# Kernel optimization log

Measured on AMD Instinct MI355X. Metric: run time of the kernel, lower is better.

The kernel has to match this reference:

```python
import jax, jax.numpy as jnp
import numpy as np

N_NODES = 50000


def _gcn_norm(edge_index, num_nodes):
    """Add self-loops and compute symmetric GCN normalization per edge.
    Returns (src, dst, norm) with src/dst of length E + N."""
    loop = jnp.arange(num_nodes, dtype=edge_index.dtype)
    src = jnp.concatenate([edge_index[0], loop])
    dst = jnp.concatenate([edge_index[1], loop])
    ones = jnp.ones(dst.shape[0], dtype=jnp.float32)
    deg = jax.ops.segment_sum(ones, dst, num_segments=num_nodes)
    dinv = jnp.where(deg > 0, jax.lax.rsqrt(deg), 0.0)
    norm = dinv[src] * dinv[dst]  # [E + N]
    return src, dst, norm


def _gcn_conv(x, src, dst, norm, W, b, num_nodes):
    h = x @ W                                # [N, out]
    msg = h[src] * norm[:, None]             # gather + scale, [E+N, out]
    out = jax.ops.segment_sum(msg, dst, num_segments=num_nodes)  # scatter-add
    return out + b


def setup_inputs() -> dict:
    key = jax.random.key(0)
    ks = jax.random.split(key, 10)
    F, H = 128, 128
    x = jax.random.normal(ks[0], (N_NODES, F), dtype=jnp.float32)
    edge_index = jax.random.randint(ks[1], (2, 800000), 0, N_NODES, dtype=jnp.int64)
    def glorot(k, fan_in, fan_out):
        s = (6.0 / (fan_in + fan_out)) ** 0.5
        return jax.random.uniform(k, (fan_in, fan_out), jnp.float32, -s, s)
    return {
        "x": x,
        "edge_index": edge_index,
        "W1": glorot(ks[2], F, H), "b1": jnp.zeros((H,), jnp.float32),
        "W2": glorot(ks[3], H, H), "b2": jnp.zeros((H,), jnp.float32),
        "W3": glorot(ks[4], H, H), "b3": jnp.zeros((H,), jnp.float32),
        "W4": glorot(ks[5], H, F), "b4": jnp.zeros((F,), jnp.float32),
    }


def reference(x, edge_index, W1, b1, W2, b2, W3, b3, W4, b4):
    n = x.shape[0]
    src, dst, norm = _gcn_norm(edge_index, n)  # same edges for all 4 layers
    h = jax.nn.relu(_gcn_conv(x, src, dst, norm, W1, b1, n))
    h = jax.nn.relu(_gcn_conv(h, src, dst, norm, W2, b2, n))
    h = jax.nn.relu(_gcn_conv(h, src, dst, norm, W3, b3, n))
    h = jax.nn.relu(_gcn_conv(h, src, dst, norm, W4, b4, n))
    return h
```

## Files before the change

kernel.cpp:

```cpp
#include <hip/hip_runtime.h>
#include <hip/hip_fp16.h>

typedef __attribute__((ext_vector_type(8))) _Float16 half8;
typedef __attribute__((ext_vector_type(4))) float f32x4;

static __device__ __forceinline__ half8 as_half8(uint4 u) {
    union { uint4 u; half8 h; } c; c.u = u; return c.h;
}


__global__ void prep_k(int* __restrict__ cnt, const float* __restrict__ x,
                       __half* __restrict__ Xh, int N) {
    int stride = gridDim.x * 256;
    int tid = blockIdx.x * 256 + threadIdx.x;
    for (int i = tid; i < 12544; i += stride) ((int4*)cnt)[i] = make_int4(0, 0, 0, 0);
    int nOut = N * 16;
    const float4* x4 = (const float4*)x;
    uint4* o4 = (uint4*)Xh;
    for (int i = tid; i < nOut; i += stride) {
        float4 f0 = x4[i * 2 + 0];
        float4 f1 = x4[i * 2 + 1];
        __half2 h0 = __floats2half2_rn(f0.x, f0.y);
        __half2 h1 = __floats2half2_rn(f0.z, f0.w);
        __half2 h2 = __floats2half2_rn(f1.x, f1.y);
        __half2 h3 = __floats2half2_rn(f1.z, f1.w);
        uint4 o;
        o.x = *(unsigned int*)&h0;
        o.y = *(unsigned int*)&h1;
        o.z = *(unsigned int*)&h2;
        o.w = *(unsigned int*)&h3;
        o4[i] = o;
    }
}

__global__ void hist_k(const int* __restrict__ dst, int* __restrict__ cnt, int E) {
    int e4 = blockIdx.x * 256 + threadIdx.x;
    int nE4 = E >> 2;
    if (e4 < nE4) {
        int4 d = ((const int4*)dst)[e4];
        atomicAdd(&cnt[d.x], 1);
        atomicAdd(&cnt[d.y], 1);
        atomicAdd(&cnt[d.z], 1);
        atomicAdd(&cnt[d.w], 1);
    } else if (e4 == nE4) {
        for (int e = nE4 * 4; e < E; ++e) atomicAdd(&cnt[dst[e]], 1);
    }
}

__global__ void bsum_k(const int* __restrict__ cnt, int* __restrict__ bsum,
                       float* __restrict__ dinv, int n) {
    int b = blockIdx.x, tid = threadIdx.x;
    int base = b * 1024 + tid * 4;
    int4 v = make_int4(0, 0, 0, 0);
    if (base + 3 < n) v = *(const int4*)(cnt + base);
    else {
        if (base + 0 < n) v.x = cnt[base + 0];
        if (base + 1 < n) v.y = cnt[base + 1];
        if (base + 2 < n) v.z = cnt[base + 2];
    }
    if (base + 3 < n) {
        float4 dv;
        dv.x = rsqrtf((float)v.x + 1.0f);
        dv.y = rsqrtf((float)v.y + 1.0f);
        dv.z = rsqrtf((float)v.z + 1.0f);
        dv.w = rsqrtf((float)v.w + 1.0f);
        *(float4*)(dinv + base) = dv;
    } else {
        if (base + 0 < n) dinv[base + 0] = rsqrtf((float)v.x + 1.0f);
        if (base + 1 < n) dinv[base + 1] = rsqrtf((float)v.y + 1.0f);
        if (base + 2 < n) dinv[base + 2] = rsqrtf((float)v.z + 1.0f);
    }
    int s = v.x + v.y + v.z + v.w;
#pragma unroll
    for (int off = 32; off; off >>= 1) s += __shfl_xor(s, off, 64);
    __shared__ int wsh[4];
    if ((tid & 63) == 0) wsh[tid >> 6] = s;
    __syncthreads();
    if (tid == 0) bsum[b] = wsh[0] + wsh[1] + wsh[2] + wsh[3];
}

__global__ void bscan_k(const int* __restrict__ bsum, int* __restrict__ boffs, int nb) {
    int tid = threadIdx.x;
    int lane = tid & 63, wid = tid >> 6;
    int s = (tid < nb) ? bsum[tid] : 0;
    int incl = s;
#pragma unroll
    for (int off = 1; off < 64; off <<= 1) {
        int t = __shfl_up(incl, off, 64);
        if (lane >= off) incl += t;
    }
    __shared__ int wsh[4];
    if (lane == 63) wsh[wid] = incl;
    __syncthreads();
    int woff = 0;
    for (int w = 0; w < wid; ++w) woff += wsh[w];
    if (tid < nb) boffs[tid] = woff + incl - s;
}

__global__ void rowscan_k(const int* __restrict__ cnt, const int* __restrict__ boffs,
                          int* __restrict__ rowptr, int n) {
    int b = blockIdx.x, tid = threadIdx.x;
    int lane = tid & 63, wid = tid >> 6;
    int base = b * 1024 + tid * 4;
    int4 v = make_int4(0, 0, 0, 0);
    if (base + 3 < n) v = *(const int4*)(cnt + base);
    else {
        if (base + 0 < n) v.x = cnt[base + 0];
        if (base + 1 < n) v.y = cnt[base + 1];
        if (base + 2 < n) v.z = cnt[base + 2];
    }
    int s = v.x + v.y + v.z + v.w;
    int incl = s;
#pragma unroll
    for (int off = 1; off < 64; off <<= 1) {
        int t = __shfl_up(incl, off, 64);
        if (lane >= off) incl += t;
    }
    __shared__ int wsh[4];
    if (lane == 63) wsh[wid] = incl;
    __syncthreads();
    int woff = boffs[b];
    for (int w = 0; w < wid; ++w) woff += wsh[w];
    int e0 = woff + incl - s;
    int o0 = e0 + v.x, o1 = o0 + v.y, o2 = o1 + v.z, o3 = o2 + v.w;
    if (base + 0 < n) rowptr[base + 1] = o0;
    if (base + 1 < n) rowptr[base + 2] = o1;
    if (base + 2 < n) rowptr[base + 3] = o2;
    if (base + 3 < n) rowptr[base + 4] = o3;
    if (b == 0 && tid == 0) rowptr[0] = 0;
}

__global__ void copy_k(const int* __restrict__ rowptr, int* __restrict__ cursor, int n4) {
    int i = blockIdx.x * 256 + threadIdx.x;
    if (i < n4) ((int4*)cursor)[i] = ((const int4*)rowptr)[i];
}

__global__ void fill_k(const int* __restrict__ src, const int* __restrict__ dst,
                       const float* __restrict__ dinv,
                       int* __restrict__ cursor, unsigned int* __restrict__ edata, int E) {
    int e4 = blockIdx.x * 256 + threadIdx.x;
    int nE4 = E >> 2;
    if (e4 < nE4) {
        int4 d = ((const int4*)dst)[e4];
        int4 s = ((const int4*)src)[e4];
        int ds[4] = {d.x, d.y, d.z, d.w};
        int ss[4] = {s.x, s.y, s.z, s.w};
#pragma unroll
        for (int j = 0; j < 4; ++j) {
            int pos = atomicAdd(&cursor[ds[j]], 1);
            float w = dinv[ss[j]] * dinv[ds[j]];
            unsigned short wh = __half_as_ushort(__float2half(w));
            edata[pos] = ((unsigned int)ss[j] << 16) | (unsigned int)wh;
        }
    } else if (e4 == nE4) {
        for (int e = nE4 * 4; e < E; ++e) {
            int d = dst[e], s = src[e];
            int pos = atomicAdd(&cursor[d], 1);
            float w = dinv[s] * dinv[d];
            unsigned short wh = __half_as_ushort(__float2half(w));
            edata[pos] = ((unsigned int)s << 16) | (unsigned int)wh;
        }
    }
}

__global__ void wshuf_k(const float* __restrict__ W0, const float* __restrict__ W1,
                        const float* __restrict__ W2, const float* __restrict__ W3,
                        uint4* __restrict__ Wshuf) {
    int gid = blockIdx.x * 256 + threadIdx.x;
    int layer = gid >> 11;
    int tid2 = gid & 2047;
    int ks = tid2 >> 9;
    int rem = tid2 & 511;
    int ct = rem >> 6;
    int lane = rem & 63;
    const float* W = (layer == 0) ? W0 : (layer == 1) ? W1 : (layer == 2) ? W2 : W3;
    int col = ct * 16 + (lane & 15);
    int k0 = ks * 32 + (lane >> 4) * 8;
    __half h[8];
#pragma unroll
    for (int j = 0; j < 8; ++j) h[j] = __float2half(W[(k0 + j) * 128 + col]);
    uint4 o;
    o.x = *(unsigned int*)&h[0];
    o.y = *(unsigned int*)&h[2];
    o.z = *(unsigned int*)&h[4];
    o.w = *(unsigned int*)&h[6];
    Wshuf[gid] = o;
}


__global__ __launch_bounds__(256) void gemm_k(const __half* __restrict__ Xh,
                                              const uint4* __restrict__ Wsh,
                                              __half* __restrict__ Hh, int N) {
    __shared__ uint4 bsh[2048];
    int tid = threadIdx.x;
#pragma unroll
    for (int i = 0; i < 8; ++i) bsh[i * 256 + tid] = Wsh[i * 256 + tid];
    __syncthreads();

    int lane = tid & 63;
    int wv = tid >> 6;
    int rbase = blockIdx.x * 256 + wv * 64;
    int lr = lane & 15;
    int lk = lane >> 4;

    const uint4* X4 = (const uint4*)Xh;

    f32x4 acc[4][8];
#pragma unroll
    for (int rt = 0; rt < 4; ++rt)
#pragma unroll
        for (int ct = 0; ct < 8; ++ct) acc[rt][ct] = (f32x4){0.f, 0.f, 0.f, 0.f};

#pragma unroll
    for (int ks = 0; ks < 4; ++ks) {
        half8 a[4];
#pragma unroll
        for (int rt = 0; rt < 4; ++rt) {
            int row = rbase + rt * 16 + lr;
            uint4 u = (row < N) ? X4[(size_t)row * 16 + ks * 4 + lk]
                                : make_uint4(0, 0, 0, 0);
            a[rt] = as_half8(u);
        }
#pragma unroll
        for (int ct = 0; ct < 8; ++ct) {
            half8 b = as_half8(bsh[(ks * 8 + ct) * 64 + lane]);
#pragma unroll
            for (int rt = 0; rt < 4; ++rt) {
                acc[rt][ct] = __builtin_amdgcn_mfma_f32_16x16x32_f16(a[rt], b, acc[rt][ct], 0, 0, 0);
            }
        }
    }

#pragma unroll
    for (int rt = 0; rt < 4; ++rt) {
        int row0 = rbase + rt * 16 + lk * 4;
#pragma unroll
        for (int ct = 0; ct < 8; ++ct) {
            int col = ct * 16 + lr;
            f32x4 v = acc[rt][ct];
#pragma unroll
            for (int r = 0; r < 4; ++r) {
                int row = row0 + r;
                if (row < N) Hh[(size_t)row * 128 + col] = __float2half(v[r]);
            }
        }
    }
}

__device__ __forceinline__ void acc8(float* a, uint4 v, float w) {
    unsigned int u[4] = {v.x, v.y, v.z, v.w};
#pragma unroll
    for (int j = 0; j < 4; ++j) {
        __half2 h = *(__half2*)&u[j];
        float2 f = __half22float2(h);
        a[2 * j + 0] = fmaf(f.x, w, a[2 * j + 0]);
        a[2 * j + 1] = fmaf(f.y, w, a[2 * j + 1]);
    }
}

template <bool F16OUT>
__global__ __launch_bounds__(256) void gather_agg_k(
        const __half* __restrict__ Hh, const int* __restrict__ rowptr,
        const unsigned int* __restrict__ edata, const float* __restrict__ dinv,
        const float* __restrict__ b, void* __restrict__ out, int N) {
    int t = blockIdx.x * 256 + threadIdx.x;
    int i = t >> 4;
    if (i >= N) return;
    int lane = t & 15;
    const uint4* H4 = (const uint4*)Hh;

    float dn = dinv[i];
    float sn = dn * dn;

    float a[8] = {};
    uint4 hi = H4[(size_t)i * 16 + lane];
    acc8(a, hi, sn);

    int p0 = rowptr[i];
    int p1 = rowptr[i + 1];
    int p = p0;
    for (; p + 4 <= p1; p += 4) {
        unsigned int e0 = edata[p + 0];
        unsigned int e1 = edata[p + 1];
        unsigned int e2 = edata[p + 2];
        unsigned int e3 = edata[p + 3];
        uint4 v0 = H4[(size_t)(e0 >> 16) * 16 + lane];
        uint4 v1 = H4[(size_t)(e1 >> 16) * 16 + lane];
        uint4 v2 = H4[(size_t)(e2 >> 16) * 16 + lane];
        uint4 v3 = H4[(size_t)(e3 >> 16) * 16 + lane];
        float w0 = __half2float(__ushort_as_half((unsigned short)(e0 & 0xffffu)));
        float w1 = __half2float(__ushort_as_half((unsigned short)(e1 & 0xffffu)));
        float w2 = __half2float(__ushort_as_half((unsigned short)(e2 & 0xffffu)));
        float w3 = __half2float(__ushort_as_half((unsigned short)(e3 & 0xffffu)));
        acc8(a, v0, w0);
        acc8(a, v1, w1);
        acc8(a, v2, w2);
        acc8(a, v3, w3);
    }
    for (; p < p1; ++p) {
        unsigned int e = edata[p];
        uint4 v = H4[(size_t)(e >> 16) * 16 + lane];
        float w = __half2float(__ushort_as_half((unsigned short)(e & 0xffffu)));
        acc8(a, v, w);
    }

    const float4* b4 = (const float4*)b;
    float4 bb0 = b4[lane * 2 + 0];
    float4 bb1 = b4[lane * 2 + 1];
    float r[8];
    r[0] = fmaxf(a[0] + bb0.x, 0.f);
    r[1] = fmaxf(a[1] + bb0.y, 0.f);
    r[2] = fmaxf(a[2] + bb0.z, 0.f);
    r[3] = fmaxf(a[3] + bb0.w, 0.f);
    r[4] = fmaxf(a[4] + bb1.x, 0.f);
    r[5] = fmaxf(a[5] + bb1.y, 0.f);
    r[6] = fmaxf(a[6] + bb1.z, 0.f);
    r[7] = fmaxf(a[7] + bb1.w, 0.f);

    if (F16OUT) {
        __half2 h0 = __floats2half2_rn(r[0], r[1]);
        __half2 h1 = __floats2half2_rn(r[2], r[3]);
        __half2 h2 = __floats2half2_rn(r[4], r[5]);
        __half2 h3 = __floats2half2_rn(r[6], r[7]);
        uint4 o;
        o.x = *(unsigned int*)&h0;
        o.y = *(unsigned int*)&h1;
        o.z = *(unsigned int*)&h2;
        o.w = *(unsigned int*)&h3;
        ((uint4*)out)[(size_t)i * 16 + lane] = o;
    } else {
        float4* orow = (float4*)((float*)out + (size_t)i * 128);
        orow[lane * 2 + 0] = make_float4(r[0], r[1], r[2], r[3]);
        orow[lane * 2 + 1] = make_float4(r[4], r[5], r[6], r[7]);
    }
}


extern "C" void kernel_launch(void* const* d_in, const int* in_sizes, int n_in,
                              void* d_out, int out_size, void* d_ws, size_t ws_size,
                              hipStream_t stream) {
    const float* x = (const float*)d_in[0];
    const int* ei = (const int*)d_in[1];
    const int E = in_sizes[1] / 2;
    const int* srcI = ei;
    const int* dstI = ei + E;
    const float* b[4] = {(const float*)d_in[3], (const float*)d_in[5],
                         (const float*)d_in[7], (const float*)d_in[9]};
    const int N = in_sizes[0] / 128;

    int* iws = (int*)d_ws;
    int* cnt = iws;
    int* cursor = iws + 50176;
    int* rowptr = iws + 100352;
    float* dinv = (float*)(iws + 150528);
    int* bsum = iws + 200704;
    int* boffs = iws + 200768;
    unsigned int* edata = (unsigned int*)(iws + 200832);
    int edEnd = 200832 + ((E + 3) & ~3);
    uint4* Wshuf = (uint4*)(iws + edEnd);
    int wsEnd = edEnd + 32768;
    __half* Xh = (__half*)(iws + wsEnd);
    __half* Hh = (__half*)(iws + wsEnd + (size_t)N * 64);

    dim3 blk(256);
    int gE4 = ((E >> 2) + 1 + 255) / 256;
    int NB = (N + 1023) / 1024;
    int gCopy = ((N + 3) / 4 + 255) / 256;
    int gGemm = (N + 255) / 256;
    int gGather = (N * 16 + 255) / 256;

    prep_k<<<1024, blk, 0, stream>>>(cnt, x, Xh, N);
    hist_k<<<gE4, blk, 0, stream>>>(dstI, cnt, E);
    bsum_k<<<NB, blk, 0, stream>>>(cnt, bsum, dinv, N);
    bscan_k<<<1, blk, 0, stream>>>(bsum, boffs, NB);
    rowscan_k<<<NB, blk, 0, stream>>>(cnt, boffs, rowptr, N);
    copy_k<<<gCopy, blk, 0, stream>>>(rowptr, cursor, (N + 3) / 4);
    fill_k<<<gE4, blk, 0, stream>>>(srcI, dstI, dinv, cursor, edata, E);
    wshuf_k<<<32, blk, 0, stream>>>((const float*)d_in[2], (const float*)d_in[4],
                                    (const float*)d_in[6], (const float*)d_in[8], Wshuf);

    const __half* in = Xh;
    for (int l = 0; l < 4; ++l) {
        gemm_k<<<gGemm, blk, 0, stream>>>(in, Wshuf + l * 2048, Hh, N);
        if (l == 3) {
            gather_agg_k<false><<<gGather, blk, 0, stream>>>(Hh, rowptr, edata, dinv, b[l], d_out, N);
        } else {
            gather_agg_k<true><<<gGather, blk, 0, stream>>>(Hh, rowptr, edata, dinv, b[l], Xh, N);
            in = Xh;
        }
    }
}
```

Baseline: 272.8 us.

## Replace atomic CSR fill with histogram ranks, striped scatter, and column-chunked gather

The histogram kernel now records each edge's atomic rank, so a non-atomic pass can compute each edge's CSR position from rowptr plus rank. A separate 8-stripe scatter then writes edata, which removes the second round of atomics and the cursor copy. The gather kernel is rearranged so each block covers 128 nodes and one of 8 feature-column chunks, with 2 threads per node. This is meant to keep accesses to H in cache and cut the cost of the random row gathers. In exchange it adds extra rank/pos/payload arrays, reads pos and payload 8 times in the scatter, and reads edge lists 8 times in the gather.

After: 466.0 us. 70.8% more time.

```diff
diff --git a/kernel.cpp b/kernel.cpp
--- a/kernel.cpp
+++ b/kernel.cpp
@@ -33,17 +33,20 @@
     }
 }
 
-__global__ void hist_k(const int* __restrict__ dst, int* __restrict__ cnt, int E) {
+__global__ void hist_rank_k(const int* __restrict__ dst, int* __restrict__ cnt,
+                            int* __restrict__ rank, int E) {
     int e4 = blockIdx.x * 256 + threadIdx.x;
     int nE4 = E >> 2;
     if (e4 < nE4) {
         int4 d = ((const int4*)dst)[e4];
-        atomicAdd(&cnt[d.x], 1);
-        atomicAdd(&cnt[d.y], 1);
-        atomicAdd(&cnt[d.z], 1);
-        atomicAdd(&cnt[d.w], 1);
+        int4 r;
+        r.x = atomicAdd(&cnt[d.x], 1);
+        r.y = atomicAdd(&cnt[d.y], 1);
+        r.z = atomicAdd(&cnt[d.z], 1);
+        r.w = atomicAdd(&cnt[d.w], 1);
+        ((int4*)rank)[e4] = r;
     } else if (e4 == nE4) {
-        for (int e = nE4 * 4; e < E; ++e) atomicAdd(&cnt[dst[e]], 1);
+        for (int e = nE4 * 4; e < E; ++e) rank[e] = atomicAdd(&cnt[dst[e]], 1);
     }
 }
 
@@ -130,35 +133,61 @@
     if (b == 0 && tid == 0) rowptr[0] = 0;
 }
 
-__global__ void copy_k(const int* __restrict__ rowptr, int* __restrict__ cursor, int n4) {
-    int i = blockIdx.x * 256 + threadIdx.x;
-    if (i < n4) ((int4*)cursor)[i] = ((const int4*)rowptr)[i];
-}
-
-__global__ void fill_k(const int* __restrict__ src, const int* __restrict__ dst,
-                       const float* __restrict__ dinv,
-                       int* __restrict__ cursor, unsigned int* __restrict__ edata, int E) {
+__global__ void pospay_k(const int* __restrict__ src, const int* __restrict__ dst,
+                         const int* __restrict__ rank, const int* __restrict__ rowptr,
+                         const float* __restrict__ dinv,
+                         int* __restrict__ pos, unsigned int* __restrict__ payload, int E) {
     int e4 = blockIdx.x * 256 + threadIdx.x;
     int nE4 = E >> 2;
     if (e4 < nE4) {
         int4 d = ((const int4*)dst)[e4];
         int4 s = ((const int4*)src)[e4];
+        int4 r = ((const int4*)rank)[e4];
         int ds[4] = {d.x, d.y, d.z, d.w};
         int ss[4] = {s.x, s.y, s.z, s.w};
+        int rs[4] = {r.x, r.y, r.z, r.w};
+        int4 po;
+        uint4 py;
+        int* pop = &po.x;
+        unsigned int* pyp = &py.x;
 #pragma unroll
         for (int j = 0; j < 4; ++j) {
-            int pos = atomicAdd(&cursor[ds[j]], 1);
+            pop[j] = rowptr[ds[j]] + rs[j];
             float w = dinv[ss[j]] * dinv[ds[j]];
             unsigned short wh = __half_as_ushort(__float2half(w));
-            edata[pos] = ((unsigned int)ss[j] << 16) | (unsigned int)wh;
-        }
+            pyp[j] = ((unsigned int)ss[j] << 16) | (unsigned int)wh;
+        }
+        ((int4*)pos)[e4] = po;
+        ((uint4*)payload)[e4] = py;
     } else if (e4 == nE4) {
         for (int e = nE4 * 4; e < E; ++e) {
             int d = dst[e], s = src[e];
-            int pos = atomicAdd(&cursor[d], 1);
+            pos[e] = rowptr[d] + rank[e];
             float w = dinv[s] * dinv[d];
             unsigned short wh = __half_as_ushort(__float2half(w));
-            edata[pos] = ((unsigned int)s << 16) | (unsigned int)wh;
+            payload[e] = ((unsigned int)s << 16) | (unsigned int)wh;
+        }
+    }
+}
+
+__global__ void scatter8_k(const int* __restrict__ pos, const unsigned int* __restrict__ payload,
+                           unsigned int* __restrict__ edata, int E, int S) {
+    int stripe = blockIdx.x & 7;
+    int lo = stripe * S;
+    int hi = min(E, lo + S);
+    int e4 = (blockIdx.x >> 3) * 256 + threadIdx.x;
+    int nE4 = E >> 2;
+    if (e4 < nE4) {
+        int4 p = ((const int4*)pos)[e4];
+        uint4 y = ((const uint4*)payload)[e4];
+        if (p.x >= lo && p.x < hi) edata[p.x] = y.x;
+        if (p.y >= lo && p.y < hi) edata[p.y] = y.y;
+        if (p.z >= lo && p.z < hi) edata[p.z] = y.z;
+        if (p.w >= lo && p.w < hi) edata[p.w] = y.w;
+    } else if (e4 == nE4) {
+        for (int e = nE4 * 4; e < E; ++e) {
+            int p = pos[e];
+            if (p >= lo && p < hi) edata[p] = payload[e];
         }
     }
 }
@@ -262,19 +291,21 @@
 __global__ __launch_bounds__(256) void gather_agg_k(
         const __half* __restrict__ Hh, const int* __restrict__ rowptr,
         const unsigned int* __restrict__ edata, const float* __restrict__ dinv,
-        const float* __restrict__ b, void* __restrict__ out, int N) {
-    int t = blockIdx.x * 256 + threadIdx.x;
-    int i = t >> 4;
+        const float* __restrict__ bias, void* __restrict__ out, int N) {
+    int c = blockIdx.x & 7;
+    int nb = blockIdx.x >> 3;
+    int t = threadIdx.x;
+    int i = nb * 128 + (t >> 1);
     if (i >= N) return;
-    int lane = t & 15;
+    int h = t & 1;
+    int fo = c * 2 + h;
     const uint4* H4 = (const uint4*)Hh;
 
     float dn = dinv[i];
     float sn = dn * dn;
 
     float a[8] = {};
-    uint4 hi = H4[(size_t)i * 16 + lane];
-    acc8(a, hi, sn);
+    acc8(a, H4[(size_t)i * 16 + fo], sn);
 
     int p0 = rowptr[i];
     int p1 = rowptr[i + 1];
@@ -284,10 +315,10 @@
         unsigned int e1 = edata[p + 1];
         unsigned int e2 = edata[p + 2];
         unsigned int e3 = edata[p + 3];
-        uint4 v0 = H4[(size_t)(e0 >> 16) * 16 + lane];
-        uint4 v1 = H4[(size_t)(e1 >> 16) * 16 + lane];
-        uint4 v2 = H4[(size_t)(e2 >> 16) * 16 + lane];
-        uint4 v3 = H4[(size_t)(e3 >> 16) * 16 + lane];
+        uint4 v0 = H4[(size_t)(e0 >> 16) * 16 + fo];
+        uint4 v1 = H4[(size_t)(e1 >> 16) * 16 + fo];
+        uint4 v2 = H4[(size_t)(e2 >> 16) * 16 + fo];
+        uint4 v3 = H4[(size_t)(e3 >> 16) * 16 + fo];
         float w0 = __half2float(__ushort_as_half((unsigned short)(e0 & 0xffffu)));
         float w1 = __half2float(__ushort_as_half((unsigned short)(e1 & 0xffffu)));
         float w2 = __half2float(__ushort_as_half((unsigned short)(e2 & 0xffffu)));
@@ -299,14 +330,14 @@
     }
     for (; p < p1; ++p) {
         unsigned int e = edata[p];
-        uint4 v = H4[(size_t)(e >> 16) * 16 + lane];
+        uint4 v = H4[(size_t)(e >> 16) * 16 + fo];
         float w = __half2float(__ushort_as_half((unsigned short)(e & 0xffffu)));
         acc8(a, v, w);
     }
 
-    const float4* b4 = (const float4*)b;
-    float4 bb0 = b4[lane * 2 + 0];
-    float4 bb1 = b4[lane * 2 + 1];
+    const float4* b4 = (const float4*)bias;
+    float4 bb0 = b4[c * 4 + h * 2 + 0];
+    float4 bb1 = b4[c * 4 + h * 2 + 1];
     float r[8];
     r[0] = fmaxf(a[0] + bb0.x, 0.f);
     r[1] = fmaxf(a[1] + bb0.y, 0.f);
@@ -327,11 +358,11 @@
         o.y = *(unsigned int*)&h1;
         o.z = *(unsigned int*)&h2;
         o.w = *(unsigned int*)&h3;
-        ((uint4*)out)[(size_t)i * 16 + lane] = o;
+        ((uint4*)out)[(size_t)i * 16 + fo] = o;
     } else {
-        float4* orow = (float4*)((float*)out + (size_t)i * 128);
-        orow[lane * 2 + 0] = make_float4(r[0], r[1], r[2], r[3]);
-        orow[lane * 2 + 1] = make_float4(r[4], r[5], r[6], r[7]);
+        float* orow = (float*)out + (size_t)i * 128 + c * 16 + h * 8;
+        *(float4*)(orow + 0) = make_float4(r[0], r[1], r[2], r[3]);
+        *(float4*)(orow + 4) = make_float4(r[4], r[5], r[6], r[7]);
     }
 }
 
@@ -347,35 +378,37 @@
     const float* b[4] = {(const float*)d_in[3], (const float*)d_in[5],
                          (const float*)d_in[7], (const float*)d_in[9]};
     const int N = in_sizes[0] / 128;
+    const int Ea = (E + 3) & ~3;
 
     int* iws = (int*)d_ws;
     int* cnt = iws;
-    int* cursor = iws + 50176;
-    int* rowptr = iws + 100352;
-    float* dinv = (float*)(iws + 150528);
-    int* bsum = iws + 200704;
-    int* boffs = iws + 200768;
-    unsigned int* edata = (unsigned int*)(iws + 200832);
-    int edEnd = 200832 + ((E + 3) & ~3);
-    uint4* Wshuf = (uint4*)(iws + edEnd);
-    int wsEnd = edEnd + 32768;
-    __half* Xh = (__half*)(iws + wsEnd);
-    __half* Hh = (__half*)(iws + wsEnd + (size_t)N * 64);
+    int* rowptr = iws + 50176;
+    float* dinv = (float*)(iws + 100352);
+    int* bsum = iws + 150528;
+    int* boffs = iws + 150592;
+    int* rank = iws + 150656;
+    int* pos = rank + Ea;
+    unsigned int* payload = (unsigned int*)(pos + Ea);
+    unsigned int* edata = payload + Ea;
+    uint4* Wshuf = (uint4*)(edata + Ea);
+    int* wsEnd = (int*)(Wshuf + 8192);
+    __half* Xh = (__half*)wsEnd;
+    __half* Hh = (__half*)(wsEnd + (size_t)N * 64);
 
     dim3 blk(256);
     int gE4 = ((E >> 2) + 1 + 255) / 256;
     int NB = (N + 1023) / 1024;
-    int gCopy = ((N + 3) / 4 + 255) / 256;
     int gGemm = (N + 255) / 256;
-    int gGather = (N * 16 + 255) / 256;
+    int gGather = ((N + 127) / 128) * 8;
+    int S = (((E + 7) / 8) + 31) & ~31;
 
     prep_k<<<1024, blk, 0, stream>>>(cnt, x, Xh, N);
-    hist_k<<<gE4, blk, 0, stream>>>(dstI, cnt, E);
+    hist_rank_k<<<gE4, blk, 0, stream>>>(dstI, cnt, rank, E);
     bsum_k<<<NB, blk, 0, stream>>>(cnt, bsum, dinv, N);
     bscan_k<<<1, blk, 0, stream>>>(bsum, boffs, NB);
     rowscan_k<<<NB, blk, 0, stream>>>(cnt, boffs, rowptr, N);
-    copy_k<<<gCopy, blk, 0, stream>>>(rowptr, cursor, (N + 3) / 4);
-    fill_k<<<gE4, blk, 0, stream>>>(srcI, dstI, dinv, cursor, edata, E);
+    pospay_k<<<gE4, blk, 0, stream>>>(srcI, dstI, rank, rowptr, dinv, pos, payload, E);
+    scatter8_k<<<gE4 * 8, blk, 0, stream>>>(pos, payload, edata, E, S);
     wshuf_k<<<32, blk, 0, stream>>>((const float*)d_in[2], (const float*)d_in[4],
                                     (const float*)d_in[6], (const float*)d_in[8], Wshuf);
 
```
